# Kernel optimization log

Measured on AMD Instinct MI355X. Metric: run time of the kernel, lower is better.

Reference implementation:

```python
import jax, jax.numpy as jnp
import numpy as np

SIGMA_LOW = 0.2
SIGMA_HIGH = 0.01
DT = 0.1


def _gauss_kernel(sigma):
    # tw always uses sigma_low for its range, as in the original __init__
    tw = jnp.arange(-3.0 * SIGMA_LOW, 3.0 * SIGMA_LOW, 0.001 * DT, dtype=jnp.float32)  # 12000 taps
    g = jnp.exp(-0.5 * (tw / sigma) ** 2)
    return g / jnp.sum(g)


def _same_corr_fft(x, w):
    """tf.nn.conv1d(x, w_shared, stride=1, padding='SAME') where the same 1-D
    kernel w is applied to every channel independently (shared-weight depthwise).
    x: (1, T, C) NWC, w: (K,). FFT-based since K=12000 taps."""
    T = x.shape[1]
    K = w.shape[0]
    N = T + K - 1                      # full linear correlation length
    pad_left = (K - 1) // 2            # TF SAME left padding
    Xf = jnp.fft.rfft(x, n=N, axis=1)
    Wf = jnp.fft.rfft(w[::-1], n=N)    # flip kernel: correlation via convolution
    z = jnp.fft.irfft(Xf * Wf[None, :, None], n=N, axis=1)  # (1, N, C)
    start = K - 1 - pad_left           # offset of SAME output inside full result
    return jax.lax.dynamic_slice_in_dim(z, start, T, axis=1)


def setup_inputs() -> dict:
    key = jax.random.key(0)
    firings = jax.random.normal(key, (1, 100000, 512), dtype=jnp.float32)
    sel_idx = jnp.arange(256, dtype=jnp.int32)  # static boolean mask -> gather indices
    return {
        "firings": firings,
        "gauss_low": _gauss_kernel(SIGMA_LOW),
        "gauss_high": _gauss_kernel(SIGMA_HIGH),
        "sel_idx": sel_idx,
    }


def reference(firings, gauss_low, gauss_high, sel_idx):
    # boolean_mask(firings, mask, axis=2) -> channel gather
    sel = jnp.take(firings, sel_idx, axis=2)              # (1, T, Csel)
    low = _same_corr_fft(sel, gauss_low)                  # low-pass component
    filt = sel - low + jnp.mean(low)                      # high-pass + restore global mean
    return _same_corr_fft(filt, gauss_high)               # smooth with narrow Gaussian
```

## Files before the change

### kernel.cpp

```cpp
#include <hip/hip_runtime.h>
#include <hip/hip_bf16.h>

#define T_LEN   100000
#define C_SEL   256
#define C_IN    512
#define KLOW    12000
#define B1      50
#define NB1     2000
#define ND1     2001
#define NW1     241
#define ND2E    5003
#define WH_OFF  5500
#define KH      1001
#define NR2     8
#define NGX     626
#define NPG     5
#define NWG     (NGX*NPG)
#define MLEN    5000

typedef __attribute__((ext_vector_type(4))) float f32x4;

__global__ __launch_bounds__(256) void kA_prep(const float* __restrict__ x,
                                               const int* __restrict__ sel,
                                               const float* __restrict__ wlow,
                                               const float* __restrict__ whigh,
                                               float* __restrict__ S,
                                               float* __restrict__ W1,
                                               float* __restrict__ musum,
                                               float* __restrict__ cwh){
  if (blockIdx.x < NB1){
    __shared__ f32x4 red[4][64];
    int jb = blockIdx.x;
    int tid = threadIdx.x;
    int c4 = tid & 63;
    int w  = tid >> 6;
    int s0 = sel[4*c4+0], s1 = sel[4*c4+1], s2 = sel[4*c4+2], s3 = sel[4*c4+3];
    bool contig = (s0 == 4*c4) && (s1 == 4*c4+1) && (s2 == 4*c4+2) && (s3 == 4*c4+3);
    bool allc = __all(contig);
    f32x4 acc = {0.f, 0.f, 0.f, 0.f};
    const float* rowb = x + (size_t)jb*(B1*C_IN);
    if (allc){
      for (int i = w; i < B1; i += 4)
        acc += *reinterpret_cast<const f32x4*>(rowb + (size_t)i*C_IN + 4*c4);
    } else {
      for (int i = w; i < B1; i += 4){
        const float* r = rowb + (size_t)i*C_IN;
        f32x4 v = { r[s0], r[s1], r[s2], r[s3] };
        acc += v;
      }
    }
    red[w][c4] = acc;
    __syncthreads();
    if (tid < 64){
      f32x4 s = red[0][tid] + red[1][tid] + red[2][tid] + red[3][tid];
      *reinterpret_cast<f32x4*>(S + (size_t)jb*C_SEL + 4*tid) = s;
    }
  } else {
    int m1 = threadIdx.x;
    if (m1 == 0){
      musum[0] = 0.f;
      float run = 0.f;
      cwh[0] = 0.f;
      for (int j = 0; j < KH; ++j){ run += whigh[WH_OFF + j]; cwh[j+1] = run; }
    }
    if (m1 < NW1){
      float s = 0.f;
      int kbase = 50*m1 - 1;
      for (int off = 0; off < 50; ++off){
        int k = kbase + off;
        if (k >= 0 && k < KLOW) s += wlow[k];
      }
      W1[m1] = s * (1.0f/50.0f);
    }
  }
}

__global__ __launch_bounds__(256) void kB_lowd(const float* __restrict__ S,
                                               const float* __restrict__ W1,
                                               float* __restrict__ lowd,
                                               float* __restrict__ musum){
  __shared__ float w1s[NW1];
  int tid = threadIdx.x;
  if (tid < NW1) w1s[tid] = W1[tid];
  __syncthreads();
  int jd   = blockIdx.x*4 + (tid >> 6);
  int lane = tid & 63;
  if (jd >= ND1) return;
  int lo = 120 - jd;  if (lo < 0)   lo = 0;
  int hi = 2119 - jd; if (hi > 240) hi = 240;
  f32x4 acc = {0.f, 0.f, 0.f, 0.f};
  for (int m1 = lo; m1 <= hi; ++m1){
    int jb = jd + m1 - 120;
    acc += w1s[m1] * *reinterpret_cast<const f32x4*>(S + (size_t)jb*C_SEL + 4*lane);
  }
  *reinterpret_cast<f32x4*>(lowd + (size_t)jd*C_SEL + 4*lane) = acc;
  float t = acc.x + acc.y + acc.z + acc.w;
  for (int off = 32; off > 0; off >>= 1) t += __shfl_down(t, off);
  if (lane == 0){
    float ew = (jd == 0) ? 25.5f : ((jd == ND1-1) ? 24.5f : 50.f);
    atomicAdd(musum, ew*t);
  }
}

template<bool FAST>
__device__ __forceinline__ void conv_core4(const float* __restrict__ x,
                                           const float* __restrict__ whs,
                                           int m0, int p, int lane,
                                           int s0, int s1, int s2, int s3,
                                           bool allc, f32x4* acc){
  float wr[8];
  if (FAST){
    const float* base = x + (size_t)(20*m0 + p)*C_IN + 4*lane;
    f32x4 vb[8];
    #pragma unroll
    for (int q = 0; q < 8; ++q)
      vb[q] = *reinterpret_cast<const f32x4*>(base + (size_t)q*(20*C_IN));
    #pragma unroll
    for (int q = 0; q < 58; ++q){
      wr[q & 7] = (q <= 50) ? whs[20*q + p] : 0.f;
      f32x4 v = vb[q & 7];
      if (q + 8 < 58)
        vb[q & 7] = *reinterpret_cast<const f32x4*>(base + (size_t)(q+8)*(20*C_IN));
      #pragma unroll
      for (int r = 0; r < NR2; ++r){
        int u = q - r;
        if (u >= 0 && u <= 50) acc[r] += wr[u & 7]*v;
      }
    }
  } else {
    #pragma unroll
    for (int q = 0; q < 58; ++q){
      int m = m0 + q;
      f32x4 v = {0.f, 0.f, 0.f, 0.f};
      if (m >= 0 && m < MLEN){
        const float* row = x + (size_t)(20*m + p)*C_IN;
        if (allc) v = *reinterpret_cast<const f32x4*>(row + 4*lane);
        else      v = f32x4{ row[s0], row[s1], row[s2], row[s3] };
      }
      wr[q & 7] = (q <= 50) ? whs[20*q + p] : 0.f;
      #pragma unroll
      for (int r = 0; r < NR2; ++r){
        int u = q - r;
        if (u >= 0 && u <= 50) acc[r] += wr[u & 7]*v;
      }
    }
  }
}

__global__ __launch_bounds__(256) void kC_conv(const float* __restrict__ x,
                                               const int* __restrict__ sel,
                                               const float* __restrict__ whigh,
                                               float* __restrict__ outp){
  __shared__ float whs[1024];
  __shared__ f32x4 red[4][NR2][64];
  int tid = threadIdx.x;
  for (int i = tid; i < 1024; i += 256){
    int j = i - 1;
    whs[i] = (j >= 0 && j < KH) ? whigh[WH_OFF + j] : 0.f;
  }
  int lin = blockIdx.x;
  int xcd = lin & 7, pos = lin >> 3;
  int wg  = (xcd < 2 ? xcd*392 : 784 + (xcd - 2)*391) + pos;
  int xg  = wg % NGX;
  int pgb = wg / NGX;
  int lane = tid & 63;
  int w    = tid >> 6;
  int p    = pgb*4 + w;
  int jo0  = xg * NR2;
  int m0   = jo0 - 26;
  int s0 = sel[4*lane+0], s1 = sel[4*lane+1], s2 = sel[4*lane+2], s3 = sel[4*lane+3];
  bool allc = __all((s0 == 4*lane) && (s1 == 4*lane+1) && (s2 == 4*lane+2) && (s3 == 4*lane+3));
  __syncthreads();
  f32x4 acc[NR2];
  #pragma unroll
  for (int r = 0; r < NR2; ++r) acc[r] = f32x4{0.f, 0.f, 0.f, 0.f};
  if (m0 >= 0 && m0 + 57 < MLEN && allc)
       conv_core4<true >(x, whs, m0, p, lane, s0, s1, s2, s3, allc, acc);
  else conv_core4<false>(x, whs, m0, p, lane, s0, s1, s2, s3, allc, acc);
  #pragma unroll
  for (int r = 0; r < NR2; ++r) red[w][r][lane] = acc[r];
  __syncthreads();

  int r  = tid >> 5;
  int jo = jo0 + r;
  if (jo < ND2E){
    #pragma unroll
    for (int k = 0; k < 2; ++k){
      int j = ((tid & 31) << 1) + k;
      f32x4 a = red[0][r][j] + red[1][r][j] + red[2][r][j] + red[3][r][j];
      *reinterpret_cast<f32x4*>(outp + ((size_t)pgb*ND2E + jo)*C_SEL + 4*j) = a;
    }
  }
}

__global__ __launch_bounds__(256) void kC_red(const float* __restrict__ outp,
                                              const float* __restrict__ cwh,
                                              const float* __restrict__ lowd,
                                              const float* __restrict__ musum,
                                              float* __restrict__ outd){
  int tid = threadIdx.x;
  int jo  = blockIdx.x*4 + (tid >> 6);
  int j   = tid & 63;
  if (jo >= ND2E) return;
  f32x4 a = {0.f, 0.f, 0.f, 0.f};
  #pragma unroll
  for (int pg = 0; pg < NPG; ++pg)
    a += *reinterpret_cast<const f32x4*>(outp + ((size_t)pg*ND2E + jo)*C_SEL + 4*j);
  float mu = musum[0] * (1.0f/((float)T_LEN*(float)C_SEL));
  int tn = 20*(jo - 1);
  int jmin = 499 - tn;             if (jmin < 0) jmin = 0;
  int jmax = T_LEN - 1 + 499 - tn; if (jmax > 1000) jmax = 1000;
  float s = cwh[jmax + 1] - cwh[jmin];
  int tc = tn < 0 ? 0 : (tn > T_LEN-1 ? T_LEN-1 : tn);
  int jd = tc/50, rr = tc - 50*jd;
  float fr = rr*(1.f/50.f);
  f32x4 l0 = *reinterpret_cast<const f32x4*>(lowd + (size_t)jd*C_SEL + 4*j);
  f32x4 l1 = *reinterpret_cast<const f32x4*>(lowd + (size_t)(jd+1)*C_SEL + 4*j);
  f32x4 lo = l0 + (l1 - l0)*fr;
  *reinterpret_cast<f32x4*>(outd + (size_t)jo*C_SEL + 4*j) = a + (mu - lo)*s;
}

__global__ __launch_bounds__(256) void kD_interp(const float* __restrict__ outd,
                                                 float* __restrict__ out){
  int tid  = threadIdx.x;
  int lane = tid & 63;
  int w    = tid >> 6;
  int t0   = blockIdx.x*8;
  #pragma unroll
  for (int k = 0; k < 2; ++k){
    int t = t0 + w + 4*k;
    int jo = t/20, rr = t - jo*20;
    float a = rr*(1.f/20.f);
    const float* b = outd + (size_t)jo*C_SEL + 4*lane;
    f32x4 p0 = *reinterpret_cast<const f32x4*>(b);
    f32x4 p1 = *reinterpret_cast<const f32x4*>(b +   C_SEL);
    f32x4 p2 = *reinterpret_cast<const f32x4*>(b + 2*C_SEL);
    f32x4 p3 = *reinterpret_cast<const f32x4*>(b + 3*C_SEL);
    f32x4 m = p1 + 0.5f*a*((p2 - p0)
            + a*((2.f*p0 - 5.f*p1 + 4.f*p2 - p3)
            + a*(3.f*(p1 - p2) + p3 - p0)));
    *reinterpret_cast<f32x4*>(out + (size_t)t*C_SEL + 4*lane) = m;
  }
}

extern "C" void kernel_launch(void* const* d_in, const int* in_sizes, int n_in,
                              void* d_out, int out_size, void* d_ws, size_t ws_size,
                              hipStream_t stream){
  const float* firings = (const float*)d_in[0];
  const float* glow    = (const float*)d_in[1];
  const float* ghigh   = (const float*)d_in[2];
  const int*   sel     = (const int*)d_in[3];
  float* out = (float*)d_out;
  float* ws  = (float*)d_ws;

  float* W1    = ws;
  float* musum = ws + 256;
  float* cwh   = ws + 320;
  float* S     = ws + 2048;
  float* lowd  = ws + 514048;
  float* outd  = ws + 1026304;
  float* outp  = ws + 2307072;

  hipLaunchKernelGGL(kA_prep,  dim3(NB1+1),    dim3(256), 0, stream,
                     firings, sel, glow, ghigh, S, W1, musum, cwh);
  hipLaunchKernelGGL(kB_lowd,  dim3(501),      dim3(256), 0, stream, S, W1, lowd, musum);
  hipLaunchKernelGGL(kC_conv,  dim3(NWG),      dim3(256), 0, stream,
                     firings, sel, ghigh, outp);
  hipLaunchKernelGGL(kC_red,   dim3(1251),     dim3(256), 0, stream,
                     outp, cwh, lowd, musum, outd);
  hipLaunchKernelGGL(kD_interp,dim3(T_LEN/8),  dim3(256), 0, stream, outd, out);
}
```

Baseline: 450.9 us.

## Double outputs per workgroup in high-pass conv and hoist taps to scalar registers

Each workgroup of the narrow-Gaussian convolution now computes 16 output rows instead of 8, halving the grid. Each input row loaded is therefore reused across more accumulators and the 50-row halo is amortised over more outputs. The 51 tap weights are loaded once into wave-uniform scalar registers via readfirstlane, so they are no longer reloaded from LDS for each row. The LDS reduction is split into four chunks with extra barriers to keep shared memory small, and the XCD workgroup mapping is re-tuned. In exchange it raises register pressure (16 f32x4 accumulators plus 51 weights) and drops the explicit prefetch ring, which may lower occupancy and latency hiding.

Result: slower. 474.1 us (+5.2%).

```diff
diff --git a/kernel.cpp b/kernel.cpp
--- a/kernel.cpp
+++ b/kernel.cpp
@@ -12,13 +12,18 @@
 #define ND2E    5003
 #define WH_OFF  5500
 #define KH      1001
-#define NR2     8
-#define NGX     626
+#define NR2     16
+#define NQ      (NR2+50)
+#define NGX     313
 #define NPG     5
 #define NWG     (NGX*NPG)
 #define MLEN    5000
 
 typedef __attribute__((ext_vector_type(4))) float f32x4;
+
+__device__ __forceinline__ float rf(float x){
+  return __int_as_float(__builtin_amdgcn_readfirstlane(__float_as_int(x)));
+}
 
 __global__ __launch_bounds__(256) void kA_prep(const float* __restrict__ x,
                                                const int* __restrict__ sel,
@@ -103,33 +108,27 @@
 }
 
 template<bool FAST>
-__device__ __forceinline__ void conv_core4(const float* __restrict__ x,
+__device__ __forceinline__ void conv_core5(const float* __restrict__ x,
                                            const float* __restrict__ whs,
                                            int m0, int p, int lane,
                                            int s0, int s1, int s2, int s3,
                                            bool allc, f32x4* acc){
-  float wr[8];
   if (FAST){
+    float wt_[51];
+    #pragma unroll
+    for (int u = 0; u < 51; ++u) wt_[u] = rf(whs[20*u + p]);
     const float* base = x + (size_t)(20*m0 + p)*C_IN + 4*lane;
-    f32x4 vb[8];
     #pragma unroll
-    for (int q = 0; q < 8; ++q)
-      vb[q] = *reinterpret_cast<const f32x4*>(base + (size_t)q*(20*C_IN));
-    #pragma unroll
-    for (int q = 0; q < 58; ++q){
-      wr[q & 7] = (q <= 50) ? whs[20*q + p] : 0.f;
-      f32x4 v = vb[q & 7];
-      if (q + 8 < 58)
-        vb[q & 7] = *reinterpret_cast<const f32x4*>(base + (size_t)(q+8)*(20*C_IN));
+    for (int q = 0; q < NQ; ++q){
+      f32x4 v = *reinterpret_cast<const f32x4*>(base + (size_t)q*(20*C_IN));
       #pragma unroll
       for (int r = 0; r < NR2; ++r){
         int u = q - r;
-        if (u >= 0 && u <= 50) acc[r] += wr[u & 7]*v;
+        if (u >= 0 && u <= 50) acc[r] += wt_[u]*v;
       }
     }
   } else {
-    #pragma unroll
-    for (int q = 0; q < 58; ++q){
+    for (int q = 0; q < NQ; ++q){
       int m = m0 + q;
       f32x4 v = {0.f, 0.f, 0.f, 0.f};
       if (m >= 0 && m < MLEN){
@@ -137,11 +136,10 @@
         if (allc) v = *reinterpret_cast<const f32x4*>(row + 4*lane);
         else      v = f32x4{ row[s0], row[s1], row[s2], row[s3] };
       }
-      wr[q & 7] = (q <= 50) ? whs[20*q + p] : 0.f;
       #pragma unroll
       for (int r = 0; r < NR2; ++r){
         int u = q - r;
-        if (u >= 0 && u <= 50) acc[r] += wr[u & 7]*v;
+        if (u >= 0 && u <= 50) acc[r] += whs[20*u + p]*v;
       }
     }
   }
@@ -152,7 +150,7 @@
                                                const float* __restrict__ whigh,
                                                float* __restrict__ outp){
   __shared__ float whs[1024];
-  __shared__ f32x4 red[4][NR2][64];
+  __shared__ f32x4 red[4][4][64];
   int tid = threadIdx.x;
   for (int i = tid; i < 1024; i += 256){
     int j = i - 1;
@@ -160,7 +158,7 @@
   }
   int lin = blockIdx.x;
   int xcd = lin & 7, pos = lin >> 3;
-  int wg  = (xcd < 2 ? xcd*392 : 784 + (xcd - 2)*391) + pos;
+  int wg  = (xcd < 5 ? xcd*196 : 980 + (xcd - 5)*195) + pos;
   int xg  = wg % NGX;
   int pgb = wg / NGX;
   int lane = tid & 63;
@@ -174,21 +172,21 @@
   f32x4 acc[NR2];
   #pragma unroll
   for (int r = 0; r < NR2; ++r) acc[r] = f32x4{0.f, 0.f, 0.f, 0.f};
-  if (m0 >= 0 && m0 + 57 < MLEN && allc)
-       conv_core4<true >(x, whs, m0, p, lane, s0, s1, s2, s3, allc, acc);
-  else conv_core4<false>(x, whs, m0, p, lane, s0, s1, s2, s3, allc, acc);
-  #pragma unroll
-  for (int r = 0; r < NR2; ++r) red[w][r][lane] = acc[r];
-  __syncthreads();
-
-  int r  = tid >> 5;
-  int jo = jo0 + r;
-  if (jo < ND2E){
+  if (m0 >= 0 && jo0 + NR2 - 1 + 24 < MLEN && allc)
+       conv_core5<true >(x, whs, m0, p, lane, s0, s1, s2, s3, allc, acc);
+  else conv_core5<false>(x, whs, m0, p, lane, s0, s1, s2, s3, allc, acc);
+
+  #pragma unroll
+  for (int ch = 0; ch < 4; ++ch){
+    if (ch) __syncthreads();
     #pragma unroll
-    for (int k = 0; k < 2; ++k){
-      int j = ((tid & 31) << 1) + k;
-      f32x4 a = red[0][r][j] + red[1][r][j] + red[2][r][j] + red[3][r][j];
-      *reinterpret_cast<f32x4*>(outp + ((size_t)pgb*ND2E + jo)*C_SEL + 4*j) = a;
+    for (int rr = 0; rr < 4; ++rr) red[w][rr][lane] = acc[ch*4 + rr];
+    __syncthreads();
+    int r2 = tid >> 6;
+    int jo = jo0 + ch*4 + r2;
+    if (jo < ND2E){
+      f32x4 a = red[0][r2][lane] + red[1][r2][lane] + red[2][r2][lane] + red[3][r2][lane];
+      *reinterpret_cast<f32x4*>(outp + ((size_t)pgb*ND2E + jo)*C_SEL + 4*lane) = a;
     }
   }
 }
```
